# Performance work log

Measured on AMD Instinct MI355X. Metric: run time of the kernel, lower is better.

Reference implementation:

```python
import jax, jax.numpy as jnp
import numpy as np

B, C, H, W = 8, 128, 64, 64


def setup_inputs() -> dict:
    key = jax.random.key(0)
    ks = jax.random.split(key, 4)
    s = 1.0 / np.sqrt(C)
    return {
        "x": jax.random.normal(ks[0], (B, C, H, W), dtype=jnp.float32),
        "Wq": jax.random.normal(ks[1], (C, C), dtype=jnp.float32) * s,
        "bq": jnp.zeros((C,), dtype=jnp.float32),
        "Wk": jax.random.normal(ks[2], (C, C), dtype=jnp.float32) * s,
        "bk": jnp.zeros((C,), dtype=jnp.float32),
        "Wv": jax.random.normal(ks[3], (C, C), dtype=jnp.float32) * s,
        "bv": jnp.zeros((C,), dtype=jnp.float32),
    }


def reference(x, Wq, bq, Wk, bk, Wv, bv):
    b, c, h, w = x.shape
    xf = x.reshape(b, c, h * w)  # [B, C, N]
    # 1x1 convs are per-pixel CxC matmuls (weight[out,in] contracted over in)
    q = jnp.einsum("oc,bcn->bon", Wq, xf) + bq[None, :, None]
    k = jnp.einsum("oc,bcn->bon", Wk, xf) + bk[None, :, None]
    v = jnp.einsum("oc,bcn->bon", Wv, xf) + bv[None, :, None]
    scale = 1.0 / jnp.sqrt(jnp.asarray(c, dtype=x.dtype))
    attn = jnp.einsum("bcn,bcm->bnm", q, k) * scale  # [B, N, N]
    attn = jax.nn.softmax(attn, axis=-1)
    out = jnp.einsum("bnm,bcm->bcn", attn, v)  # [B, C, N]
    return out.reshape(b, c, h, w) + x
```

## Files before the change

### kernel.cpp

```cpp
#include <hip/hip_runtime.h>

#define B_ 8
#define C_ 128
#define N_ 4096
#define SCALE_L2E 0.1275174462578437f

typedef __attribute__((ext_vector_type(8))) short short8;
typedef __attribute__((ext_vector_type(4))) short short4v;
typedef __attribute__((ext_vector_type(4))) float f32x4;

__device__ inline float b2f(unsigned short u) {
    union { unsigned int i; float f; } v; v.i = ((unsigned int)u) << 16; return v.f;
}
__device__ inline unsigned short f2b(float f) {
    unsigned int x = __float_as_uint(f);
    return (unsigned short)((x + 0x7FFFu + ((x >> 16) & 1u)) >> 16);
}

__device__ inline void gld_lds16(const void* g, void* l) {
    __builtin_amdgcn_global_load_lds(
        (const __attribute__((address_space(1))) unsigned int*)g,
        (__attribute__((address_space(3))) unsigned int*)l, 16, 0, 0);
}

__global__ __launch_bounds__(256) void qkv_mfma(
    const float* __restrict__ x,
    const float* __restrict__ Wq, const float* __restrict__ bq,
    const float* __restrict__ Wk, const float* __restrict__ bk,
    const float* __restrict__ Wv, const float* __restrict__ bv,
    float* __restrict__ q, unsigned short* __restrict__ kTs,
    unsigned short* __restrict__ vS)
{
    __shared__ __align__(16) short Xs[64 * 128];
    __shared__ __align__(16) float Obuf[64 * 132];

    const int t    = threadIdx.x;
    const int w    = t >> 6;
    const int lane = t & 63;
    const int l15  = lane & 15;
    const int quad = lane >> 4;

    const int b  = blockIdx.x & 7;
    const int n0 = (blockIdx.x >> 3) * 64;
    const long base = (long)b * C_ * N_;

    auto load_af = [&](const float* __restrict__ W, short8 (&af)[2][4]) {
        #pragma unroll
        for (int ot = 0; ot < 2; ++ot) {
            const int o = 32 * w + 16 * ot + l15;
            #pragma unroll
            for (int ks = 0; ks < 4; ++ks) {
                const float4 a0 = *(const float4*)(const void*)(W + o * C_ + ks * 32 + quad * 8);
                const float4 a1 = *(const float4*)(const void*)(W + o * C_ + ks * 32 + quad * 8 + 4);
                short8 f;
                f[0] = (short)f2b(a0.x); f[1] = (short)f2b(a0.y);
                f[2] = (short)f2b(a0.z); f[3] = (short)f2b(a0.w);
                f[4] = (short)f2b(a1.x); f[5] = (short)f2b(a1.y);
                f[6] = (short)f2b(a1.z); f[7] = (short)f2b(a1.w);
                af[ot][ks] = f;
            }
        }
    };

    auto mfma_pass = [&](const short8 (&af)[2][4], f32x4 (&acc)[2][4]) {
        #pragma unroll
        for (int ot = 0; ot < 2; ++ot)
            #pragma unroll
            for (int nt = 0; nt < 4; ++nt)
                acc[ot][nt] = (f32x4){0.f, 0.f, 0.f, 0.f};
        #pragma unroll
        for (int nt = 0; nt < 4; ++nt) {
            const int n = nt * 16 + l15;
            short8 bx[4];
            #pragma unroll
            for (int ks = 0; ks < 4; ++ks)
                bx[ks] = *(const short8*)(const void*)(Xs + n * 128 + (((ks * 4 + quad) ^ l15) << 3));
            #pragma unroll
            for (int ot = 0; ot < 2; ++ot)
                #pragma unroll
                for (int ks = 0; ks < 4; ++ks)
                    acc[ot][nt] = __builtin_amdgcn_mfma_f32_16x16x32_bf16(af[ot][ks], bx[ks], acc[ot][nt], 0, 0, 0);
        }
    };

    short8 afA[2][4], afB[2][4];
    load_af(Wq, afA);

    #pragma unroll
    for (int it = 0; it < 8; ++it) {
        const int c  = (t >> 4) + it * 16;
        const int n4 = (t & 15) * 4;
        const float4 xv = *(const float4*)(const void*)(x + base + (long)c * N_ + n0 + n4);
        const int bc = c >> 3, cl = c & 7;
        Xs[(n4 + 0) * 128 + ((bc ^ ((n4 + 0) & 15)) << 3) + cl] = (short)f2b(xv.x);
        Xs[(n4 + 1) * 128 + ((bc ^ ((n4 + 1) & 15)) << 3) + cl] = (short)f2b(xv.y);
        Xs[(n4 + 2) * 128 + ((bc ^ ((n4 + 2) & 15)) << 3) + cl] = (short)f2b(xv.z);
        Xs[(n4 + 3) * 128 + ((bc ^ ((n4 + 3) & 15)) << 3) + cl] = (short)f2b(xv.w);
    }
    __syncthreads();

    {
        load_af(Wv, afB);
        f32x4 acc[2][4];
        mfma_pass(afA, acc);
        #pragma unroll
        for (int ot = 0; ot < 2; ++ot)
            #pragma unroll
            for (int r = 0; r < 4; ++r) {
                const int o = 32 * w + 16 * ot + quad * 4 + r;
                const float bb = bq[o];
                #pragma unroll
                for (int nt = 0; nt < 4; ++nt)
                    q[base + (long)o * N_ + n0 + nt * 16 + l15] = (acc[ot][nt][r] + bb) * SCALE_L2E;
            }
    }

    {
        load_af(Wk, afA);
        f32x4 acc[2][4];
        mfma_pass(afB, acc);
        #pragma unroll
        for (int ot = 0; ot < 2; ++ot)
            #pragma unroll
            for (int r = 0; r < 4; ++r) {
                const int o = 32 * w + 16 * ot + quad * 4 + r;
                const float bb = bv[o];
                const int sw = ((o >> 1) & 3) << 3;
                #pragma unroll
                for (int nt = 0; nt < 4; ++nt) {
                    const int n = nt * 16 + l15;
                    const int ns = (n & 32) | ((((n >> 3) & 3) << 3) ^ sw) | (n & 7);
                    vS[base + (long)o * N_ + n0 + ns] = f2b(acc[ot][nt][r] + bb);
                }
            }
    }

    {
        f32x4 acc[2][4];
        mfma_pass(afA, acc);
        #pragma unroll
        for (int ot = 0; ot < 2; ++ot)
            #pragma unroll
            for (int r = 0; r < 4; ++r) {
                const int o = 32 * w + 16 * ot + quad * 4 + r;
                const float bb = bk[o];
                #pragma unroll
                for (int nt = 0; nt < 4; ++nt) {
                    const int n = nt * 16 + l15;
                    Obuf[n * 132 + (((o >> 3) ^ l15) << 3) + (o & 7)] = acc[ot][nt][r] + bb;
                }
            }
        __syncthreads();
        const int n = t >> 2, oh = (t & 3) * 32;
        #pragma unroll
        for (int i = 0; i < 32; i += 4) {
            const float4 kv = *(const float4*)(const void*)(Obuf + n * 132 + oh + i);
            short4v s;
            s[0] = (short)f2b(kv.x); s[1] = (short)f2b(kv.y);
            s[2] = (short)f2b(kv.z); s[3] = (short)f2b(kv.w);
            *(short4v*)(void*)(kTs + base + (long)(n0 + n) * C_ + oh + i) = s;
        }
    }
}

__global__ __launch_bounds__(512, 4) void attn_mfma(
    const float* qg,
    const unsigned short* __restrict__ kTs,
    const unsigned short* __restrict__ vS,
    const float* __restrict__ xg,
    float* out)
{
    __shared__ union {
        struct {
            short K[2][2][4096];
            short V[2][2][4096];
            short Pb[2][2][32 * 40];
        } s;
        float Ot[64 * 130];
    } sm;
    __shared__ float Ls[2][2][32];
    __shared__ float linvA[64];

    const int t    = threadIdx.x;
    const int w    = t >> 6;
    const int g    = w >> 2;
    const int wq   = (w >> 1) & 1;
    const int h    = w & 1;
    const int sub  = w & 3;
    const int lane = t & 63;
    const int l15  = lane & 15;
    const int quad = lane >> 4;

    const int b  = blockIdx.x & 7;
    const int n0 = (blockIdx.x >> 3) * 64;
    const long base = (long)b * C_ * N_;

    const int query0 = n0 + 32 * wq;
    short8 qf[2][4];
    #pragma unroll
    for (int qh = 0; qh < 2; ++qh)
        #pragma unroll
        for (int ks = 0; ks < 4; ++ks) {
            short8 f;
            #pragma unroll
            for (int j = 0; j < 8; ++j) {
                const int c = ks * 32 + quad * 8 + j;
                f[j] = (short)f2b(qg[base + (long)c * N_ + query0 + qh * 16 + l15]);
            }
            qf[qh][ks] = f;
        }

    f32x4 acc[2][4];
    #pragma unroll
    for (int qh = 0; qh < 2; ++qh)
        #pragma unroll
        for (int ct = 0; ct < 4; ++ct) acc[qh][ct] = (f32x4){0.f, 0.f, 0.f, 0.f};
    f32x4 accS[2];
    accS[0] = (f32x4){0.f, 0.f, 0.f, 0.f};
    accS[1] = (f32x4){0.f, 0.f, 0.f, 0.f};
    short8 ones;
    #pragma unroll
    for (int j = 0; j < 8; ++j) ones[j] = (short)0x3F80;

    auto stage = [&](int buf, int pair) {
        const int mt = pair * 2 + g;
        const char* gK = (const char*)(kTs + base + (long)mt * 32 * C_);
        char* lK = (char*)sm.s.K[buf][g];
        char* lV = (char*)sm.s.V[buf][g];
        #pragma unroll
        for (int jj = 0; jj < 2; ++jj) {
            const int d = sub * 2048 + jj * 1024;
            gld_lds16(gK + d + lane * 16, lK + d);
            const int dv = d + lane * 16;
            const int c  = dv >> 6;
            gld_lds16((const char*)(vS + base + (long)c * N_ + mt * 32) + (dv & 63), lV + d);
        }
    };

    stage(0, 0);
    for (int i = 0; i < 64; ++i) {
        if (i < 63) {
            stage((i + 1) & 1, i + 1);
            asm volatile("s_waitcnt vmcnt(4)" ::: "memory");
        } else {
            asm volatile("s_waitcnt vmcnt(0)" ::: "memory");
        }
        __builtin_amdgcn_s_barrier();

        const int buf = i & 1;
        const short* Kb = sm.s.K[buf][g];
        const short* Vb = sm.s.V[buf][g];

        short8 kf[4];
        #pragma unroll
        for (int ks = 0; ks < 4; ++ks)
            kf[ks] = *(const short8*)(const void*)(Kb + (h * 16 + l15) * 128 + (((ks * 4 + quad) ^ l15) << 3));
        f32x4 sc[2];
        sc[0] = (f32x4){0.f, 0.f, 0.f, 0.f};
        sc[1] = (f32x4){0.f, 0.f, 0.f, 0.f};
        __builtin_amdgcn_s_setprio(1);
        #pragma unroll
        for (int qh = 0; qh < 2; ++qh)
            #pragma unroll
            for (int ks = 0; ks < 4; ++ks)
                sc[qh] = __builtin_amdgcn_mfma_f32_16x16x32_bf16(qf[qh][ks], kf[ks], sc[qh], 0, 0, 0);
        __builtin_amdgcn_s_setprio(0);

        short* Pw = sm.s.Pb[g][wq];
        #pragma unroll
        for (int qh = 0; qh < 2; ++qh)
            #pragma unroll
            for (int r = 0; r < 4; ++r)
                Pw[(qh * 16 + quad * 4 + r) * 40 + h * 16 + l15] = (short)f2b(exp2f(sc[qh][r]));

        asm volatile("s_waitcnt lgkmcnt(0)" ::: "memory");
        __builtin_amdgcn_s_barrier();
        __builtin_amdgcn_sched_barrier(0);

        const short8 pf0 = *(const short8*)(const void*)(Pw + (l15) * 40 + quad * 8);
        const short8 pf1 = *(const short8*)(const void*)(Pw + (16 + l15) * 40 + quad * 8);
        __builtin_amdgcn_s_setprio(1);
        if (h == 0) {
            accS[0] = __builtin_amdgcn_mfma_f32_16x16x32_bf16(pf0, ones, accS[0], 0, 0, 0);
            accS[1] = __builtin_amdgcn_mfma_f32_16x16x32_bf16(pf1, ones, accS[1], 0, 0, 0);
        }
        #pragma unroll
        for (int ct = 0; ct < 4; ++ct) {
            const int ch = h * 64 + ct * 16 + l15;
            const short8 vf = *(const short8*)(const void*)(Vb + ch * 32 + ((quad ^ ((l15 >> 1) & 3)) << 3));
            acc[0][ct] = __builtin_amdgcn_mfma_f32_16x16x32_bf16(pf0, vf, acc[0][ct], 0, 0, 0);
            acc[1][ct] = __builtin_amdgcn_mfma_f32_16x16x32_bf16(pf1, vf, acc[1][ct], 0, 0, 0);
        }
        __builtin_amdgcn_s_setprio(0);
        __builtin_amdgcn_s_barrier();
    }

    if (h == 0 && l15 == 0) {
        #pragma unroll
        for (int qh = 0; qh < 2; ++qh)
            #pragma unroll
            for (int r = 0; r < 4; ++r)
                Ls[g][wq][qh * 16 + quad * 4 + r] = accS[qh][r];
    }
    if (g == 0) {
        #pragma unroll
        for (int qh = 0; qh < 2; ++qh)
            #pragma unroll
            for (int ct = 0; ct < 4; ++ct)
                #pragma unroll
                for (int r = 0; r < 4; ++r)
                    sm.Ot[(32 * wq + qh * 16 + quad * 4 + r) * 130 + h * 64 + ct * 16 + l15] = acc[qh][ct][r];
    }
    __syncthreads();
    if (g == 1) {
        #pragma unroll
        for (int qh = 0; qh < 2; ++qh)
            #pragma unroll
            for (int ct = 0; ct < 4; ++ct)
                #pragma unroll
                for (int r = 0; r < 4; ++r)
                    sm.Ot[(32 * wq + qh * 16 + quad * 4 + r) * 130 + h * 64 + ct * 16 + l15] += acc[qh][ct][r];
    } else if (h == 0 && l15 == 0) {
        #pragma unroll
        for (int qh = 0; qh < 2; ++qh)
            #pragma unroll
            for (int r = 0; r < 4; ++r) {
                const int r32 = qh * 16 + quad * 4 + r;
                linvA[32 * wq + r32] = 1.0f / fmaxf(Ls[0][wq][r32] + Ls[1][wq][r32], 1e-20f);
            }
    }
    __syncthreads();

    const int c  = t >> 2;
    const int nh = (t & 3) * 16;
    const long gb = base + (long)c * N_ + n0 + nh;
    #pragma unroll
    for (int i = 0; i < 16; i += 4) {
        const float4 xs = *(const float4*)(const void*)(xg + gb + i);
        float4 rv;
        rv.x = sm.Ot[(nh + i + 0) * 130 + c] * linvA[nh + i + 0] + xs.x;
        rv.y = sm.Ot[(nh + i + 1) * 130 + c] * linvA[nh + i + 1] + xs.y;
        rv.z = sm.Ot[(nh + i + 2) * 130 + c] * linvA[nh + i + 2] + xs.z;
        rv.w = sm.Ot[(nh + i + 3) * 130 + c] * linvA[nh + i + 3] + xs.w;
        *(float4*)(void*)(out + gb + i) = rv;
    }
}

extern "C" void kernel_launch(void* const* d_in, const int* in_sizes, int n_in,
                              void* d_out, int out_size, void* d_ws, size_t ws_size,
                              hipStream_t stream) {
    const float* x  = (const float*)d_in[0];
    const float* Wq = (const float*)d_in[1];
    const float* bq = (const float*)d_in[2];
    const float* Wk = (const float*)d_in[3];
    const float* bk = (const float*)d_in[4];
    const float* Wv = (const float*)d_in[5];
    const float* bv = (const float*)d_in[6];
    float* out = (float*)d_out;

    const long BCN = (long)B_ * C_ * N_;
    unsigned short* kTs = (unsigned short*)d_ws;
    unsigned short* vS  = kTs + BCN;

    qkv_mfma<<<512, 256, 0, stream>>>(x, Wq, bq, Wk, bk, Wv, bv, out, kTs, vS);
    attn_mfma<<<B_ * (N_ / 64), 512, 0, stream>>>(out, kTs, vS, x, out);
}
```

Baseline: 198.2 us.

## Load K fragments directly to registers, double-buffer P, and split QKV output channels

The attention loop stops staging K through LDS. Each wave prefetches its swizzled K fragments from global memory straight into registers one iteration ahead, while V stays in double-buffered LDS and is now staged after the barrier. P gets a double buffer, which removes the trailing barrier of each iteration, and exp2 with a log2e-folded scale becomes __expf with a plain scale. The QKV kernel splits the output channels across two blocks (1024 blocks) and writes the swizzled K layout directly from registers, dropping the LDS transpose buffer. The cost is more global traffic for K per wave and a different exp path.

```diff
diff --git a/kernel.cpp b/kernel.cpp
--- a/kernel.cpp
+++ b/kernel.cpp
@@ -3,7 +3,7 @@
 #define B_ 8
 #define C_ 128
 #define N_ 4096
-#define SCALE_L2E 0.1275174462578437f
+#define SCALE 0.08838834764831845f
 
 typedef __attribute__((ext_vector_type(8))) short short8;
 typedef __attribute__((ext_vector_type(4))) short short4v;
@@ -32,7 +32,6 @@
     unsigned short* __restrict__ vS)
 {
     __shared__ __align__(16) short Xs[64 * 128];
-    __shared__ __align__(16) float Obuf[64 * 132];
 
     const int t    = threadIdx.x;
     const int w    = t >> 6;
@@ -40,50 +39,42 @@
     const int l15  = lane & 15;
     const int quad = lane >> 4;
 
-    const int b  = blockIdx.x & 7;
-    const int n0 = (blockIdx.x >> 3) * 64;
+    const int b    = blockIdx.x & 7;
+    const int rest = blockIdx.x >> 3;
+    const int oh   = rest & 1;
+    const int n0   = (rest >> 1) * 64;
     const long base = (long)b * C_ * N_;
 
-    auto load_af = [&](const float* __restrict__ W, short8 (&af)[2][4]) {
-        #pragma unroll
-        for (int ot = 0; ot < 2; ++ot) {
-            const int o = 32 * w + 16 * ot + l15;
-            #pragma unroll
-            for (int ks = 0; ks < 4; ++ks) {
-                const float4 a0 = *(const float4*)(const void*)(W + o * C_ + ks * 32 + quad * 8);
-                const float4 a1 = *(const float4*)(const void*)(W + o * C_ + ks * 32 + quad * 8 + 4);
-                short8 f;
-                f[0] = (short)f2b(a0.x); f[1] = (short)f2b(a0.y);
-                f[2] = (short)f2b(a0.z); f[3] = (short)f2b(a0.w);
-                f[4] = (short)f2b(a1.x); f[5] = (short)f2b(a1.y);
-                f[6] = (short)f2b(a1.z); f[7] = (short)f2b(a1.w);
-                af[ot][ks] = f;
-            }
+    auto load_af = [&](const float* __restrict__ W, short8 (&af)[4]) {
+        const int o = oh * 64 + 16 * w + l15;
+        #pragma unroll
+        for (int ks = 0; ks < 4; ++ks) {
+            const float4 a0 = *(const float4*)(const void*)(W + o * C_ + ks * 32 + quad * 8);
+            const float4 a1 = *(const float4*)(const void*)(W + o * C_ + ks * 32 + quad * 8 + 4);
+            short8 f;
+            f[0] = (short)f2b(a0.x); f[1] = (short)f2b(a0.y);
+            f[2] = (short)f2b(a0.z); f[3] = (short)f2b(a0.w);
+            f[4] = (short)f2b(a1.x); f[5] = (short)f2b(a1.y);
+            f[6] = (short)f2b(a1.z); f[7] = (short)f2b(a1.w);
+            af[ks] = f;
         }
     };
 
-    auto mfma_pass = [&](const short8 (&af)[2][4], f32x4 (&acc)[2][4]) {
-        #pragma unroll
-        for (int ot = 0; ot < 2; ++ot)
-            #pragma unroll
-            for (int nt = 0; nt < 4; ++nt)
-                acc[ot][nt] = (f32x4){0.f, 0.f, 0.f, 0.f};
+    auto mfma_pass = [&](const short8 (&af)[4], f32x4 (&acc)[4]) {
+        #pragma unroll
+        for (int nt = 0; nt < 4; ++nt) acc[nt] = (f32x4){0.f, 0.f, 0.f, 0.f};
         #pragma unroll
         for (int nt = 0; nt < 4; ++nt) {
             const int n = nt * 16 + l15;
-            short8 bx[4];
-            #pragma unroll
-            for (int ks = 0; ks < 4; ++ks)
-                bx[ks] = *(const short8*)(const void*)(Xs + n * 128 + (((ks * 4 + quad) ^ l15) << 3));
-            #pragma unroll
-            for (int ot = 0; ot < 2; ++ot)
-                #pragma unroll
-                for (int ks = 0; ks < 4; ++ks)
-                    acc[ot][nt] = __builtin_amdgcn_mfma_f32_16x16x32_bf16(af[ot][ks], bx[ks], acc[ot][nt], 0, 0, 0);
+            #pragma unroll
+            for (int ks = 0; ks < 4; ++ks) {
+                const short8 bx = *(const short8*)(const void*)(Xs + n * 128 + (((ks * 4 + quad) ^ l15) << 3));
+                acc[nt] = __builtin_amdgcn_mfma_f32_16x16x32_bf16(af[ks], bx, acc[nt], 0, 0, 0);
+            }
         }
     };
 
-    short8 afA[2][4], afB[2][4];
+    short8 afA[4], afB[4];
     load_af(Wq, afA);
 
     #pragma unroll
@@ -99,66 +90,54 @@
     }
     __syncthreads();
 
+    const int O0 = oh * 64 + 16 * w + quad * 4;
+
     {
         load_af(Wv, afB);
-        f32x4 acc[2][4];
+        f32x4 acc[4];
         mfma_pass(afA, acc);
         #pragma unroll
-        for (int ot = 0; ot < 2; ++ot)
-            #pragma unroll
-            for (int r = 0; r < 4; ++r) {
-                const int o = 32 * w + 16 * ot + quad * 4 + r;
-                const float bb = bq[o];
-                #pragma unroll
-                for (int nt = 0; nt < 4; ++nt)
-                    q[base + (long)o * N_ + n0 + nt * 16 + l15] = (acc[ot][nt][r] + bb) * SCALE_L2E;
-            }
+        for (int r = 0; r < 4; ++r) {
+            const int o = O0 + r;
+            const float bb = bq[o];
+            #pragma unroll
+            for (int nt = 0; nt < 4; ++nt)
+                q[base + (long)o * N_ + n0 + nt * 16 + l15] = (acc[nt][r] + bb) * SCALE;
+        }
     }
 
     {
         load_af(Wk, afA);
-        f32x4 acc[2][4];
+        f32x4 acc[4];
         mfma_pass(afB, acc);
         #pragma unroll
-        for (int ot = 0; ot < 2; ++ot)
-            #pragma unroll
-            for (int r = 0; r < 4; ++r) {
-                const int o = 32 * w + 16 * ot + quad * 4 + r;
-                const float bb = bv[o];
-                const int sw = ((o >> 1) & 3) << 3;
-                #pragma unroll
-                for (int nt = 0; nt < 4; ++nt) {
-                    const int n = nt * 16 + l15;
-                    const int ns = (n & 32) | ((((n >> 3) & 3) << 3) ^ sw) | (n & 7);
-                    vS[base + (long)o * N_ + n0 + ns] = f2b(acc[ot][nt][r] + bb);
-                }
+        for (int r = 0; r < 4; ++r) {
+            const int o = O0 + r;
+            const float bb = bv[o];
+            const int sw = ((o >> 1) & 3) << 3;
+            #pragma unroll
+            for (int nt = 0; nt < 4; ++nt) {
+                const int n = nt * 16 + l15;
+                const int ns = (n & 32) | ((((n >> 3) & 3) << 3) ^ sw) | (n & 7);
+                vS[base + (long)o * N_ + n0 + ns] = f2b(acc[nt][r] + bb);
             }
+        }
     }
 
     {
-        f32x4 acc[2][4];
+        f32x4 acc[4];
         mfma_pass(afA, acc);
-        #pragma unroll
-        for (int ot = 0; ot < 2; ++ot)
-            #pragma unroll
-            for (int r = 0; r < 4; ++r) {
-                const int o = 32 * w + 16 * ot + quad * 4 + r;
-                const float bb = bk[o];
-                #pragma unroll
-                for (int nt = 0; nt < 4; ++nt) {
-                    const int n = nt * 16 + l15;
-                    Obuf[n * 132 + (((o >> 3) ^ l15) << 3) + (o & 7)] = acc[ot][nt][r] + bb;
-                }
-            }
-        __syncthreads();
-        const int n = t >> 2, oh = (t & 3) * 32;
-        #pragma unroll
-        for (int i = 0; i < 32; i += 4) {
-            const float4 kv = *(const float4*)(const void*)(Obuf + n * 132 + oh + i);
+        const float4 bb = *(const float4*)(const void*)(bk + O0);
+        #pragma unroll
+        for (int nt = 0; nt < 4; ++nt) {
+            const int n = nt * 16 + l15;
             short4v s;
-            s[0] = (short)f2b(kv.x); s[1] = (short)f2b(kv.y);
-            s[2] = (short)f2b(kv.z); s[3] = (short)f2b(kv.w);
-            *(short4v*)(void*)(kTs + base + (long)(n0 + n) * C_ + oh + i) = s;
+            s[0] = (short)f2b(acc[nt][0] + bb.x);
+            s[1] = (short)f2b(acc[nt][1] + bb.y);
+            s[2] = (short)f2b(acc[nt][2] + bb.z);
+            s[3] = (short)f2b(acc[nt][3] + bb.w);
+            *(short4v*)(void*)(kTs + base + (long)(n0 + n) * C_
+                               + (((O0 >> 3) ^ l15) << 3) + (O0 & 7)) = s;
         }
     }
 }
@@ -172,9 +151,8 @@
 {
     __shared__ union {
         struct {
-            short K[2][2][4096];
             short V[2][2][4096];
-            short Pb[2][2][32 * 40];
+            short Pb[2][2][2][32 * 40];
         } s;
         float Ot[64 * 130];
     } sm;
@@ -222,39 +200,30 @@
     #pragma unroll
     for (int j = 0; j < 8; ++j) ones[j] = (short)0x3F80;
 
-    auto stage = [&](int buf, int pair) {
+    auto stageV = [&](int buf, int pair) {
         const int mt = pair * 2 + g;
-        const char* gK = (const char*)(kTs + base + (long)mt * 32 * C_);
-        char* lK = (char*)sm.s.K[buf][g];
         char* lV = (char*)sm.s.V[buf][g];
         #pragma unroll
         for (int jj = 0; jj < 2; ++jj) {
-            const int d = sub * 2048 + jj * 1024;
-            gld_lds16(gK + d + lane * 16, lK + d);
+            const int d  = sub * 2048 + jj * 1024;
             const int dv = d + lane * 16;
             const int c  = dv >> 6;
             gld_lds16((const char*)(vS + base + (long)c * N_ + mt * 32) + (dv & 63), lV + d);
         }
     };
 
-    stage(0, 0);
+    const unsigned short* kp = kTs + base + (long)((g * 32 + h * 16 + l15) * C_);
+    int ko[4];
+    #pragma unroll
+    for (int ks = 0; ks < 4; ++ks) ko[ks] = (((ks * 4 + quad) ^ l15) << 3);
+    short8 kf[4];
+
+    stageV(0, 0);
+    #pragma unroll
+    for (int ks = 0; ks < 4; ++ks) kf[ks] = *(const short8*)(const void*)(kp + ko[ks]);
+    kp += 64 * C_;
+
     for (int i = 0; i < 64; ++i) {
-        if (i < 63) {
-            stage((i + 1) & 1, i + 1);
-            asm volatile("s_waitcnt vmcnt(4)" ::: "memory");
-        } else {
-            asm volatile("s_waitcnt vmcnt(0)" ::: "memory");
-        }
-        __builtin_amdgcn_s_barrier();
-
-        const int buf = i & 1;
-        const short* Kb = sm.s.K[buf][g];
-        const short* Vb = sm.s.V[buf][g];
-
-        short8 kf[4];
-        #pragma unroll
-        for (int ks = 0; ks < 4; ++ks)
-            kf[ks] = *(const short8*)(const void*)(Kb + (h * 16 + l15) * 128 + (((ks * 4 + quad) ^ l15) << 3));
         f32x4 sc[2];
         sc[0] = (f32x4){0.f, 0.f, 0.f, 0.f};
         sc[1] = (f32x4){0.f, 0.f, 0.f, 0.f};
@@ -266,17 +235,28 @@
                 sc[qh] = __builtin_amdgcn_mfma_f32_16x16x32_bf16(qf[qh][ks], kf[ks], sc[qh], 0, 0, 0);
         __builtin_amdgcn_s_setprio(0);
 
-        short* Pw = sm.s.Pb[g][wq];
+        if (i < 63) {
+            #pragma unroll
+            for (int ks = 0; ks < 4; ++ks) kf[ks] = *(const short8*)(const void*)(kp + ko[ks]);
+            kp += 64 * C_;
+        }
+
+        short* Pw = sm.s.Pb[i & 1][g][wq];
         #pragma unroll
         for (int qh = 0; qh < 2; ++qh)
             #pragma unroll
             for (int r = 0; r < 4; ++r)
-                Pw[(qh * 16 + quad * 4 + r) * 40 + h * 16 + l15] = (short)f2b(exp2f(sc[qh][r]));
-
+                Pw[(qh * 16 + quad * 4 + r) * 40 + h * 16 + l15] = (short)f2b(__expf(sc[qh][r]));
+
+        if (i < 63) asm volatile("s_waitcnt vmcnt(4)" ::: "memory");
+        else        asm volatile("s_waitcnt vmcnt(0)" ::: "memory");
         asm volatile("s_waitcnt lgkmcnt(0)" ::: "memory");
         __builtin_amdgcn_s_barrier();
         __builtin_amdgcn_sched_barrier(0);
 
+        if (i < 63) stageV((i + 1) & 1, i + 1);
+
+        const short* Vb = sm.s.V[i & 1][g];
         const short8 pf0 = *(const short8*)(const void*)(Pw + (l15) * 40 + quad * 8);
         const short8 pf1 = *(const short8*)(const void*)(Pw + (16 + l15) * 40 + quad * 8);
         __builtin_amdgcn_s_setprio(1);
@@ -292,7 +272,6 @@
             acc[1][ct] = __builtin_amdgcn_mfma_f32_16x16x32_bf16(pf1, vf, acc[1][ct], 0, 0, 0);
         }
         __builtin_amdgcn_s_setprio(0);
-        __builtin_amdgcn_s_barrier();
     }
 
     if (h == 0 && l15 == 0) {
@@ -302,6 +281,7 @@
             for (int r = 0; r < 4; ++r)
                 Ls[g][wq][qh * 16 + quad * 4 + r] = accS[qh][r];
     }
+    __syncthreads();
     if (g == 0) {
         #pragma unroll
         for (int qh = 0; qh < 2; ++qh)
@@ -362,6 +342,6 @@
     unsigned short* kTs = (unsigned short*)d_ws;
     unsigned short* vS  = kTs + BCN;
 
-    qkv_mfma<<<512, 256, 0, stream>>>(x, Wq, bq, Wk, bk, Wv, bv, out, kTs, vS);
+    qkv_mfma<<<1024, 256, 0, stream>>>(x, Wq, bq, Wk, bk, Wv, bv, out, kTs, vS);
     attn_mfma<<<B_ * (N_ / 64), 512, 0, stream>>>(out, kTs, vS, x, out);
 }
```

After: 188.8 us. 4.7% less time.

## Keep P in registers, load K directly to VGPRs, drop P LDS round-trip

Applied to the files above, without the earlier changes.

Computes S transposed (K as the A operand) so each lane's exp'd scores can feed a 16x16x16 bf16 MFMA directly as the A operand, removing the P write and read through LDS and one barrier per iteration. K tiles are now loaded straight from global into registers and prefetched one step ahead, so LDS holds only V. Row sums come from a per-lane scalar accumulation of the rounded bf16 values instead of a ones-MFMA, and each wave now covers all 128 channels with an extra partial output buffer reduced at the end. The trade is more accumulator registers, half-K MFMAs, and __expf with the scale moved out of the log2e form, which could hurt occupancy.

```diff
diff --git a/kernel.cpp b/kernel.cpp
--- a/kernel.cpp
+++ b/kernel.cpp
@@ -3,7 +3,7 @@
 #define B_ 8
 #define C_ 128
 #define N_ 4096
-#define SCALE_L2E 0.1275174462578437f
+#define SCALE 0.08838834764831845f
 
 typedef __attribute__((ext_vector_type(8))) short short8;
 typedef __attribute__((ext_vector_type(4))) short short4v;
@@ -22,6 +22,21 @@
         (const __attribute__((address_space(1))) unsigned int*)g,
         (__attribute__((address_space(3))) unsigned int*)l, 16, 0, 0);
 }
+
+#if __has_builtin(__builtin_amdgcn_mfma_f32_16x16x16bf16_1k)
+__device__ inline f32x4 mfma16(short4v a, short4v b, f32x4 c) {
+    return __builtin_amdgcn_mfma_f32_16x16x16bf16_1k(a, b, c, 0, 0, 0);
+}
+#elif __has_builtin(__builtin_amdgcn_mfma_f32_16x16x16_bf16)
+__device__ inline f32x4 mfma16(short4v a, short4v b, f32x4 c) {
+    return __builtin_amdgcn_mfma_f32_16x16x16_bf16(a, b, c, 0, 0, 0);
+}
+#else
+__device__ inline f32x4 mfma16(short4v a, short4v b, f32x4 c) {
+    asm("v_mfma_f32_16x16x16_bf16 %0, %1, %2, %0" : "+v"(c) : "v"(a), "v"(b));
+    return c;
+}
+#endif
 
 __global__ __launch_bounds__(256) void qkv_mfma(
     const float* __restrict__ x,
@@ -111,7 +126,7 @@
                 const float bb = bq[o];
                 #pragma unroll
                 for (int nt = 0; nt < 4; ++nt)
-                    q[base + (long)o * N_ + n0 + nt * 16 + l15] = (acc[ot][nt][r] + bb) * SCALE_L2E;
+                    q[base + (long)o * N_ + n0 + nt * 16 + l15] = (acc[ot][nt][r] + bb) * SCALE;
             }
     }
 
@@ -170,15 +185,11 @@
     const float* __restrict__ xg,
     float* out)
 {
-    __shared__ union {
-        struct {
-            short K[2][2][4096];
-            short V[2][2][4096];
-            short Pb[2][2][32 * 40];
-        } s;
-        float Ot[64 * 130];
+    __shared__ __align__(16) union {
+        short V[2][2][4096];
+        float Ot[2][64][130];
     } sm;
-    __shared__ float Ls[2][2][32];
+    __shared__ float Ls2[2][2][4][4][16];
     __shared__ float linvA[64];
 
     const int t    = threadIdx.x;
@@ -210,124 +221,124 @@
             qf[qh][ks] = f;
         }
 
-    f32x4 acc[2][4];
+    f32x4 acc[2][8];
     #pragma unroll
     for (int qh = 0; qh < 2; ++qh)
         #pragma unroll
-        for (int ct = 0; ct < 4; ++ct) acc[qh][ct] = (f32x4){0.f, 0.f, 0.f, 0.f};
-    f32x4 accS[2];
-    accS[0] = (f32x4){0.f, 0.f, 0.f, 0.f};
-    accS[1] = (f32x4){0.f, 0.f, 0.f, 0.f};
-    short8 ones;
-    #pragma unroll
-    for (int j = 0; j < 8; ++j) ones[j] = (short)0x3F80;
-
-    auto stage = [&](int buf, int pair) {
+        for (int ct = 0; ct < 8; ++ct) acc[qh][ct] = (f32x4){0.f, 0.f, 0.f, 0.f};
+    float accSp[2] = {0.f, 0.f};
+
+    auto stageV = [&](int buf, int pair) {
         const int mt = pair * 2 + g;
-        const char* gK = (const char*)(kTs + base + (long)mt * 32 * C_);
-        char* lK = (char*)sm.s.K[buf][g];
-        char* lV = (char*)sm.s.V[buf][g];
+        char* lV = (char*)sm.V[buf][g];
         #pragma unroll
         for (int jj = 0; jj < 2; ++jj) {
-            const int d = sub * 2048 + jj * 1024;
-            gld_lds16(gK + d + lane * 16, lK + d);
+            const int d  = sub * 2048 + jj * 1024;
             const int dv = d + lane * 16;
             const int c  = dv >> 6;
             gld_lds16((const char*)(vS + base + (long)c * N_ + mt * 32) + (dv & 63), lV + d);
         }
     };
 
-    stage(0, 0);
+    const unsigned short* kp = kTs + base + (long)((g * 32 + h * 16 + l15) * C_);
+    int ko[4];
+    #pragma unroll
+    for (int ks = 0; ks < 4; ++ks) ko[ks] = (((ks * 4 + quad) ^ l15) << 3);
+    short8 kf[4];
+
+    #pragma unroll
+    for (int ks = 0; ks < 4; ++ks) kf[ks] = *(const short8*)(const void*)(kp + ko[ks]);
+    kp += 64 * C_;
+    stageV(0, 0);
+
     for (int i = 0; i < 64; ++i) {
-        if (i < 63) {
-            stage((i + 1) & 1, i + 1);
-            asm volatile("s_waitcnt vmcnt(4)" ::: "memory");
-        } else {
-            asm volatile("s_waitcnt vmcnt(0)" ::: "memory");
-        }
-        __builtin_amdgcn_s_barrier();
-
-        const int buf = i & 1;
-        const short* Kb = sm.s.K[buf][g];
-        const short* Vb = sm.s.V[buf][g];
-
-        short8 kf[4];
-        #pragma unroll
-        for (int ks = 0; ks < 4; ++ks)
-            kf[ks] = *(const short8*)(const void*)(Kb + (h * 16 + l15) * 128 + (((ks * 4 + quad) ^ l15) << 3));
         f32x4 sc[2];
         sc[0] = (f32x4){0.f, 0.f, 0.f, 0.f};
         sc[1] = (f32x4){0.f, 0.f, 0.f, 0.f};
         __builtin_amdgcn_s_setprio(1);
         #pragma unroll
-        for (int qh = 0; qh < 2; ++qh)
-            #pragma unroll
-            for (int ks = 0; ks < 4; ++ks)
-                sc[qh] = __builtin_amdgcn_mfma_f32_16x16x32_bf16(qf[qh][ks], kf[ks], sc[qh], 0, 0, 0);
+        for (int ks = 0; ks < 4; ++ks) {
+            sc[0] = __builtin_amdgcn_mfma_f32_16x16x32_bf16(kf[ks], qf[0][ks], sc[0], 0, 0, 0);
+            sc[1] = __builtin_amdgcn_mfma_f32_16x16x32_bf16(kf[ks], qf[1][ks], sc[1], 0, 0, 0);
+        }
         __builtin_amdgcn_s_setprio(0);
 
-        short* Pw = sm.s.Pb[g][wq];
-        #pragma unroll
-        for (int qh = 0; qh < 2; ++qh)
-            #pragma unroll
-            for (int r = 0; r < 4; ++r)
-                Pw[(qh * 16 + quad * 4 + r) * 40 + h * 16 + l15] = (short)f2b(exp2f(sc[qh][r]));
-
-        asm volatile("s_waitcnt lgkmcnt(0)" ::: "memory");
+        if (i < 63) {
+            #pragma unroll
+            for (int ks = 0; ks < 4; ++ks) kf[ks] = *(const short8*)(const void*)(kp + ko[ks]);
+            kp += 64 * C_;
+        }
+
+        short4v pa[2];
+        #pragma unroll
+        for (int qh = 0; qh < 2; ++qh) {
+            const float e0 = __expf(sc[qh][0]);
+            const float e1 = __expf(sc[qh][1]);
+            const float e2 = __expf(sc[qh][2]);
+            const float e3 = __expf(sc[qh][3]);
+            unsigned int w0, w1;
+            asm("v_cvt_pk_bf16_f32 %0, %1, %2" : "=v"(w0) : "v"(e0), "v"(e1));
+            asm("v_cvt_pk_bf16_f32 %0, %1, %2" : "=v"(w1) : "v"(e2), "v"(e3));
+            accSp[qh] += (__uint_as_float(w0 << 16) + __uint_as_float(w0 & 0xFFFF0000u))
+                       + (__uint_as_float(w1 << 16) + __uint_as_float(w1 & 0xFFFF0000u));
+            union { unsigned int u[2]; short4v s; } pk;
+            pk.u[0] = w0; pk.u[1] = w1;
+            pa[qh] = pk.s;
+        }
+
+        if (i < 63) asm volatile("s_waitcnt vmcnt(4)" ::: "memory");
+        else        asm volatile("s_waitcnt vmcnt(0)" ::: "memory");
         __builtin_amdgcn_s_barrier();
         __builtin_amdgcn_sched_barrier(0);
-
-        const short8 pf0 = *(const short8*)(const void*)(Pw + (l15) * 40 + quad * 8);
-        const short8 pf1 = *(const short8*)(const void*)(Pw + (16 + l15) * 40 + quad * 8);
+        if (i < 63) stageV((i + 1) & 1, i + 1);
+
+        const short* Vb = sm.V[i & 1][g];
+        const int vbk = h * 2 + (quad >> 1);
+        const int vof = (quad & 1) << 2;
         __builtin_amdgcn_s_setprio(1);
-        if (h == 0) {
-            accS[0] = __builtin_amdgcn_mfma_f32_16x16x32_bf16(pf0, ones, accS[0], 0, 0, 0);
-            accS[1] = __builtin_amdgcn_mfma_f32_16x16x32_bf16(pf1, ones, accS[1], 0, 0, 0);
-        }
-        #pragma unroll
-        for (int ct = 0; ct < 4; ++ct) {
-            const int ch = h * 64 + ct * 16 + l15;
-            const short8 vf = *(const short8*)(const void*)(Vb + ch * 32 + ((quad ^ ((l15 >> 1) & 3)) << 3));
-            acc[0][ct] = __builtin_amdgcn_mfma_f32_16x16x32_bf16(pf0, vf, acc[0][ct], 0, 0, 0);
-            acc[1][ct] = __builtin_amdgcn_mfma_f32_16x16x32_bf16(pf1, vf, acc[1][ct], 0, 0, 0);
+        #pragma unroll
+        for (int ct = 0; ct < 8; ++ct) {
+            const int ch = ct * 16 + l15;
+            const short4v vf = *(const short4v*)(const void*)(
+                Vb + ch * 32 + ((vbk ^ ((l15 >> 1) & 3)) << 3) + vof);
+            acc[0][ct] = mfma16(pa[0], vf, acc[0][ct]);
+            acc[1][ct] = mfma16(pa[1], vf, acc[1][ct]);
         }
         __builtin_amdgcn_s_setprio(0);
-        __builtin_amdgcn_s_barrier();
-    }
-
-    if (h == 0 && l15 == 0) {
+    }
+
+    __syncthreads();
+    #pragma unroll
+    for (int qh = 0; qh < 2; ++qh)
+        Ls2[g][h][quad][wq * 2 + qh][l15] = accSp[qh];
+    if (g == 0) {
         #pragma unroll
         for (int qh = 0; qh < 2; ++qh)
             #pragma unroll
-            for (int r = 0; r < 4; ++r)
-                Ls[g][wq][qh * 16 + quad * 4 + r] = accS[qh][r];
-    }
-    if (g == 0) {
-        #pragma unroll
-        for (int qh = 0; qh < 2; ++qh)
-            #pragma unroll
-            for (int ct = 0; ct < 4; ++ct)
+            for (int ct = 0; ct < 8; ++ct)
                 #pragma unroll
                 for (int r = 0; r < 4; ++r)
-                    sm.Ot[(32 * wq + qh * 16 + quad * 4 + r) * 130 + h * 64 + ct * 16 + l15] = acc[qh][ct][r];
+                    sm.Ot[h][32 * wq + qh * 16 + quad * 4 + r][ct * 16 + l15] = acc[qh][ct][r];
     }
     __syncthreads();
     if (g == 1) {
         #pragma unroll
         for (int qh = 0; qh < 2; ++qh)
             #pragma unroll
-            for (int ct = 0; ct < 4; ++ct)
+            for (int ct = 0; ct < 8; ++ct)
                 #pragma unroll
                 for (int r = 0; r < 4; ++r)
-                    sm.Ot[(32 * wq + qh * 16 + quad * 4 + r) * 130 + h * 64 + ct * 16 + l15] += acc[qh][ct][r];
-    } else if (h == 0 && l15 == 0) {
-        #pragma unroll
-        for (int qh = 0; qh < 2; ++qh)
-            #pragma unroll
-            for (int r = 0; r < 4; ++r) {
-                const int r32 = qh * 16 + quad * 4 + r;
-                linvA[32 * wq + r32] = 1.0f / fmaxf(Ls[0][wq][r32] + Ls[1][wq][r32], 1e-20f);
-            }
+                    sm.Ot[h][32 * wq + qh * 16 + quad * 4 + r][ct * 16 + l15] += acc[qh][ct][r];
+    } else if (t < 64) {
+        float s = 0.f;
+        #pragma unroll
+        for (int gg = 0; gg < 2; ++gg)
+            #pragma unroll
+            for (int hh = 0; hh < 2; ++hh)
+                #pragma unroll
+                for (int qq = 0; qq < 4; ++qq)
+                    s += Ls2[gg][hh][qq][t >> 4][t & 15];
+        linvA[t] = 1.0f / fmaxf(s, 1e-20f);
     }
     __syncthreads();
 
@@ -338,10 +349,10 @@
     for (int i = 0; i < 16; i += 4) {
         const float4 xs = *(const float4*)(const void*)(xg + gb + i);
         float4 rv;
-        rv.x = sm.Ot[(nh + i + 0) * 130 + c] * linvA[nh + i + 0] + xs.x;
-        rv.y = sm.Ot[(nh + i + 1) * 130 + c] * linvA[nh + i + 1] + xs.y;
-        rv.z = sm.Ot[(nh + i + 2) * 130 + c] * linvA[nh + i + 2] + xs.z;
-        rv.w = sm.Ot[(nh + i + 3) * 130 + c] * linvA[nh + i + 3] + xs.w;
+        rv.x = (sm.Ot[0][nh + i + 0][c] + sm.Ot[1][nh + i + 0][c]) * linvA[nh + i + 0] + xs.x;
+        rv.y = (sm.Ot[0][nh + i + 1][c] + sm.Ot[1][nh + i + 1][c]) * linvA[nh + i + 1] + xs.y;
+        rv.z = (sm.Ot[0][nh + i + 2][c] + sm.Ot[1][nh + i + 2][c]) * linvA[nh + i + 2] + xs.z;
+        rv.w = (sm.Ot[0][nh + i + 3][c] + sm.Ot[1][nh + i + 3][c]) * linvA[nh + i + 3] + xs.w;
         *(float4*)(void*)(out + gb + i) = rv;
     }
 }
```

Result: slower. 259.7 us (+31.0%).

## Load K fragments directly to registers and drop one barrier per iteration

Applied to the files above, without the earlier changes.

K tiles are now read straight from global memory into registers, prefetched one iteration ahead, instead of being staged through LDS. V staging moves after the mid-iteration barrier, and the P buffer is double-buffered so the trailing barrier per iteration can be removed. The q scale drops the log2e factor and exp2f is replaced by __expf. This cuts LDS traffic and barrier count, at the cost of more registers and uncoalesced per-lane global K loads that may add latency.

```diff
diff --git a/kernel.cpp b/kernel.cpp
--- a/kernel.cpp
+++ b/kernel.cpp
@@ -3,15 +3,12 @@
 #define B_ 8
 #define C_ 128
 #define N_ 4096
-#define SCALE_L2E 0.1275174462578437f
+#define SCALE 0.08838834764831845f
 
 typedef __attribute__((ext_vector_type(8))) short short8;
 typedef __attribute__((ext_vector_type(4))) short short4v;
 typedef __attribute__((ext_vector_type(4))) float f32x4;
 
-__device__ inline float b2f(unsigned short u) {
-    union { unsigned int i; float f; } v; v.i = ((unsigned int)u) << 16; return v.f;
-}
 __device__ inline unsigned short f2b(float f) {
     unsigned int x = __float_as_uint(f);
     return (unsigned short)((x + 0x7FFFu + ((x >> 16) & 1u)) >> 16);
@@ -111,7 +108,7 @@
                 const float bb = bq[o];
                 #pragma unroll
                 for (int nt = 0; nt < 4; ++nt)
-                    q[base + (long)o * N_ + n0 + nt * 16 + l15] = (acc[ot][nt][r] + bb) * SCALE_L2E;
+                    q[base + (long)o * N_ + n0 + nt * 16 + l15] = (acc[ot][nt][r] + bb) * SCALE;
             }
     }
 
@@ -172,9 +169,8 @@
 {
     __shared__ union {
         struct {
-            short K[2][2][4096];
             short V[2][2][4096];
-            short Pb[2][2][32 * 40];
+            short Pb[2][2][2][32 * 40];
         } s;
         float Ot[64 * 130];
     } sm;
@@ -222,39 +218,30 @@
     #pragma unroll
     for (int j = 0; j < 8; ++j) ones[j] = (short)0x3F80;
 
-    auto stage = [&](int buf, int pair) {
+    auto stageV = [&](int buf, int pair) {
         const int mt = pair * 2 + g;
-        const char* gK = (const char*)(kTs + base + (long)mt * 32 * C_);
-        char* lK = (char*)sm.s.K[buf][g];
         char* lV = (char*)sm.s.V[buf][g];
         #pragma unroll
         for (int jj = 0; jj < 2; ++jj) {
-            const int d = sub * 2048 + jj * 1024;
-            gld_lds16(gK + d + lane * 16, lK + d);
+            const int d  = sub * 2048 + jj * 1024;
             const int dv = d + lane * 16;
             const int c  = dv >> 6;
             gld_lds16((const char*)(vS + base + (long)c * N_ + mt * 32) + (dv & 63), lV + d);
         }
     };
 
-    stage(0, 0);
+    const unsigned short* kp = kTs + base + (long)((g * 32 + h * 16 + l15) * C_);
+    int ko[4];
+    #pragma unroll
+    for (int ks = 0; ks < 4; ++ks) ko[ks] = (((ks * 4 + quad) ^ l15) << 3);
+    short8 kf[4];
+
+    stageV(0, 0);
+    #pragma unroll
+    for (int ks = 0; ks < 4; ++ks) kf[ks] = *(const short8*)(const void*)(kp + ko[ks]);
+    kp += 64 * C_;
+
     for (int i = 0; i < 64; ++i) {
-        if (i < 63) {
-            stage((i + 1) & 1, i + 1);
-            asm volatile("s_waitcnt vmcnt(4)" ::: "memory");
-        } else {
-            asm volatile("s_waitcnt vmcnt(0)" ::: "memory");
-        }
-        __builtin_amdgcn_s_barrier();
-
-        const int buf = i & 1;
-        const short* Kb = sm.s.K[buf][g];
-        const short* Vb = sm.s.V[buf][g];
-
-        short8 kf[4];
-        #pragma unroll
-        for (int ks = 0; ks < 4; ++ks)
-            kf[ks] = *(const short8*)(const void*)(Kb + (h * 16 + l15) * 128 + (((ks * 4 + quad) ^ l15) << 3));
         f32x4 sc[2];
         sc[0] = (f32x4){0.f, 0.f, 0.f, 0.f};
         sc[1] = (f32x4){0.f, 0.f, 0.f, 0.f};
@@ -266,17 +253,28 @@
                 sc[qh] = __builtin_amdgcn_mfma_f32_16x16x32_bf16(qf[qh][ks], kf[ks], sc[qh], 0, 0, 0);
         __builtin_amdgcn_s_setprio(0);
 
-        short* Pw = sm.s.Pb[g][wq];
+        if (i < 63) {
+            #pragma unroll
+            for (int ks = 0; ks < 4; ++ks) kf[ks] = *(const short8*)(const void*)(kp + ko[ks]);
+            kp += 64 * C_;
+        }
+
+        short* Pw = sm.s.Pb[i & 1][g][wq];
         #pragma unroll
         for (int qh = 0; qh < 2; ++qh)
             #pragma unroll
             for (int r = 0; r < 4; ++r)
-                Pw[(qh * 16 + quad * 4 + r) * 40 + h * 16 + l15] = (short)f2b(exp2f(sc[qh][r]));
-
+                Pw[(qh * 16 + quad * 4 + r) * 40 + h * 16 + l15] = (short)f2b(__expf(sc[qh][r]));
+
+        if (i < 63) asm volatile("s_waitcnt vmcnt(4)" ::: "memory");
+        else        asm volatile("s_waitcnt vmcnt(0)" ::: "memory");
         asm volatile("s_waitcnt lgkmcnt(0)" ::: "memory");
         __builtin_amdgcn_s_barrier();
         __builtin_amdgcn_sched_barrier(0);
 
+        if (i < 63) stageV((i + 1) & 1, i + 1);
+
+        const short* Vb = sm.s.V[i & 1][g];
         const short8 pf0 = *(const short8*)(const void*)(Pw + (l15) * 40 + quad * 8);
         const short8 pf1 = *(const short8*)(const void*)(Pw + (16 + l15) * 40 + quad * 8);
         __builtin_amdgcn_s_setprio(1);
@@ -292,7 +290,6 @@
             acc[1][ct] = __builtin_amdgcn_mfma_f32_16x16x32_bf16(pf1, vf, acc[1][ct], 0, 0, 0);
         }
         __builtin_amdgcn_s_setprio(0);
-        __builtin_amdgcn_s_barrier();
     }
 
     if (h == 0 && l15 == 0) {
@@ -302,6 +299,7 @@
             for (int r = 0; r < 4; ++r)
                 Ls[g][wq][qh * 16 + quad * 4 + r] = accS[qh][r];
     }
+    __syncthreads();
     if (g == 0) {
         #pragma unroll
         for (int qh = 0; qh < 2; ++qh)
```

Result: faster. 190.9 us (-3.7%).
